# Kernel tuning notes

Hardware: AMD Instinct MI355X
Metric: run time of the kernel (lower is better)

Reference implementation:

```python
import jax, jax.numpy as jnp
import numpy as np

H = W = 56
HID = 384
B = 16

def dct_mat(N):
    # Orthonormal DCT-II matrix: X = D @ x, idct via D.T
    n = jnp.arange(N, dtype=jnp.float32)
    k = jnp.arange(N, dtype=jnp.float32)[:, None]
    D = jnp.cos(jnp.pi * (2.0 * n + 1.0) * k / (2.0 * N)) * jnp.sqrt(2.0 / N)
    D = D.at[0].multiply(1.0 / jnp.sqrt(2.0))
    return D

def setup_inputs() -> dict:
    key = jax.random.key(0)
    ks = jax.random.split(key, 16)
    s = 0.02
    return {
        "x": jax.random.normal(ks[0], (B, HID, H, W), dtype=jnp.float32),
        "freq_embed": jax.random.normal(ks[1], (H, W, HID), dtype=jnp.float32),
        "dw_w": jax.random.normal(ks[2], (HID, 1, 3, 3), dtype=jnp.float32) * s,
        "dw_b": jnp.zeros((HID,), jnp.float32),
        "lin_w": jax.random.normal(ks[3], (2 * HID, HID), dtype=jnp.float32) * s,
        "lin_b": jnp.zeros((2 * HID,), jnp.float32),
        "vel_w": jax.random.normal(ks[4], (HID, HID), dtype=jnp.float32) * s,
        "vel_b": jnp.zeros((HID,), jnp.float32),
        "tok_w": jax.random.normal(ks[5], (HID, HID), dtype=jnp.float32) * s,
        "tok_b": jnp.zeros((HID,), jnp.float32),
        "ln_g": jnp.ones((HID,), jnp.float32),
        "ln_b": jnp.zeros((HID,), jnp.float32),
        "out_w": jax.random.normal(ks[6], (HID, HID), dtype=jnp.float32) * s,
        "out_b": jnp.zeros((HID,), jnp.float32),
        "c": jnp.ones((1,), jnp.float32),
        "alpha": jnp.ones((1,), jnp.float32) * 0.1,
    }

def reference(x, freq_embed, dw_w, dw_b, lin_w, lin_b, vel_w, vel_b,
              tok_w, tok_b, ln_g, ln_b, out_w, out_b, c, alpha):
    Bn, C, Hh, Ww = x.shape
    # depthwise 3x3 conv, padding=1
    x = jax.lax.conv_general_dilated(
        x, dw_w, (1, 1), 'SAME',
        dimension_numbers=('NCHW', 'OIHW', 'NCHW'),
        feature_group_count=C) + dw_b[None, :, None, None]
    xl = jnp.transpose(x, (0, 2, 3, 1))            # [B,H,W,C]
    xz = xl @ lin_w.T + lin_b                      # [B,H,W,2C]
    xg, z = jnp.split(xz, 2, axis=-1)
    DH, DW_ = dct_mat(Hh), dct_mat(Ww)
    x_ch = jnp.transpose(xg, (0, 3, 1, 2))         # [B,C,H,W]
    x_u0 = jnp.einsum('ih,jw,bchw->bcij', DH, DW_, x_ch)
    x_vel = xg @ vel_w.T + vel_b                   # [B,H,W,C]
    x_v0 = jnp.einsum('ih,jw,bchw->bcij', DH, DW_, jnp.transpose(x_vel, (0, 3, 1, 2)))
    # decay map exp(-(n^2+m^2)) on linspace(0,pi)
    wn = jnp.linspace(0.0, jnp.pi, Hh + 1)[:Hh][:, None]
    wm = jnp.linspace(0.0, jnp.pi, Ww + 1)[:Ww][None, :]
    decay = jnp.exp(-(wn ** 2 + wm ** 2))[None, None]
    x_u0 = x_u0 * decay
    x_v0 = x_v0 * decay
    # wave modulation from freq embedding (shared across batch)
    t = jax.nn.relu(freq_embed @ tok_w.T + tok_b)  # [H,W,C]
    t = jnp.transpose(t, (2, 0, 1))[None]          # [1,C,H,W]
    eps = 1e-6
    cos_t = jnp.cos(c[0] * t)
    sin_t = jnp.sin(c[0] * t) / (c[0] + eps)
    final = cos_t * x_u0 + sin_t * (x_v0 + 0.5 * alpha[0] * x_u0)
    x_final = jnp.einsum('hi,wj,bchw->bcij', DH, DW_, final)  # IDCT2D
    y = jnp.transpose(x_final, (0, 2, 3, 1))       # [B,H,W,C]
    mu = jnp.mean(y, axis=-1, keepdims=True)
    var = jnp.mean((y - mu) ** 2, axis=-1, keepdims=True)
    yn = (y - mu) / jnp.sqrt(var + 1e-5) * ln_g + ln_b
    gated = yn * jax.nn.silu(z)                    # [B,H,W,C]
    out = gated @ out_w.T + out_b
    return jnp.transpose(out, (0, 3, 1, 2))        # [B,C,H,W]
```

## Files before the change

kernel.cpp:

```cpp
#include <hip/hip_runtime.h>
#include <math.h>

#define HH 56
#define WS_W 56
#define HWS 3136
#define CD 384
#define BB 16
#define NROW (BB*HWS)
#define SLOT ((size_t)NROW*CD)

typedef __attribute__((ext_vector_type(8))) short bf16x8;
typedef __attribute__((ext_vector_type(4))) float f32x4;

__device__ inline ushort f2bf(float v) {
  uint u = __float_as_uint(v);
  uint r = (u + 0x7fffu + ((u >> 16) & 1u)) >> 16;
  return (ushort)r;
}
__device__ inline float bf2f(ushort h) { return __uint_as_float((uint)h << 16); }

__device__ inline void gl16(const void* g, void* l) {
  __builtin_amdgcn_global_load_lds(
      (const __attribute__((address_space(1))) void*)g,
      (__attribute__((address_space(3))) void*)l,
      16, 0, 0);
}

__global__ void prep_d_k(float* __restrict__ D) {
  for (int idx = threadIdx.x; idx < HH*HH; idx += blockDim.x) {
    int k = idx / HH, n = idx % HH;
    double v = cos(3.14159265358979323846 * (2.0*n + 1.0) * k / (2.0*HH)) * sqrt(2.0/HH);
    if (k == 0) v *= 0.70710678118654752440;
    D[idx] = (float)v;
  }
}

__global__ void prep_pack_k(const float* __restrict__ Dm, ushort* __restrict__ Dpk) {
  for (int idx = threadIdx.x; idx < 2*4096; idx += 256) {
    int o = idx >> 12, e = idx & 4095;
    int mg = e >> 10, rem = e & 1023;
    int j = rem & 7, km = rem >> 3;
    int koct = km >> 4, m16 = km & 15;
    int m = mg*16 + m16, k = koct*8 + j;
    float v = 0.f;
    if (m < 56 && k < 56) v = o ? Dm[k*56 + m] : Dm[m*56 + k];
    ushort h = f2bf(v);
    Dpk[o*8192 + e] = h;
    Dpk[o*8192 + 4096 + e] = f2bf(v - bf2f(h));
  }
}

__global__ __launch_bounds__(256) void split_w_k(
    const float* __restrict__ W, ushort* __restrict__ hi,
    ushort* __restrict__ lo, int nelem) {
  int i = blockIdx.x*256 + threadIdx.x;
  if (i >= nelem) return;
  float v = W[i];
  ushort h = f2bf(v);
  hi[i] = h;
  lo[i] = f2bf(v - bf2f(h));
}

__global__ __launch_bounds__(256) void conv_k(
    const float* __restrict__ x, const float* __restrict__ dww,
    const float* __restrict__ dwb, ushort* __restrict__ xc)
{
  __shared__ float xs[3][58][33];
  __shared__ float wgt[32][9];
  __shared__ float wb[32];
  int t = threadIdx.x;
  int c0 = blockIdx.x * 32, h = blockIdx.y, b = blockIdx.z;
  for (int idx = t; idx < 1344; idx += 256) {
    int wq = idx % 14, rem = idx / 14;
    int dy = rem % 3, ch = rem / 3;
    int gh = h + dy - 1;
    float4 v = {0.f, 0.f, 0.f, 0.f};
    if (gh >= 0 && gh < HH)
      v = *(const float4*)(x + (((size_t)b*CD + c0 + ch)*HH + gh)*WS_W + wq*4);
    int wp = wq*4 + 1;
    xs[dy][wp+0][ch] = v.x;
    xs[dy][wp+1][ch] = v.y;
    xs[dy][wp+2][ch] = v.z;
    xs[dy][wp+3][ch] = v.w;
  }
  if (t < 192) {
    int e = t & 1, dy = (t >> 1) % 3, ch = t / 6;
    xs[dy][e*57][ch] = 0.f;
  }
  for (int idx = t; idx < 288; idx += 256)
    wgt[idx/9][idx%9] = dww[(size_t)(c0 + idx/9)*9 + idx%9];
  if (t < 32) wb[t] = dwb[c0 + t];
  __syncthreads();
  int ch = t & 31, wq8 = t >> 5;
  #pragma unroll
  for (int wwi = 0; wwi < 7; ++wwi) {
    int w = wwi*8 + wq8;
    float acc = wb[ch];
    #pragma unroll
    for (int dy = 0; dy < 3; ++dy)
      #pragma unroll
      for (int dx = 0; dx < 3; ++dx)
        acc = fmaf(wgt[ch][dy*3+dx], xs[dy][w+dx][ch], acc);
    size_t oi = ((size_t)b*HWS + h*WS_W + w)*CD + c0 + ch;
    ushort hh = f2bf(acc);
    xc[oi] = hh;
    xc[SLOT + oi] = f2bf(acc - bf2f(hh));
  }
}

template<int EPI>
__global__ __launch_bounds__(256) void gemm_k(
    const float* __restrict__ A, const float* __restrict__ Bw,
    const float* __restrict__ bias, float* __restrict__ out0,
    float* __restrict__ out1, const float* __restrict__ cptr)
{
  __shared__ float As[16][68];
  __shared__ float Bs[16][68];
  int t = threadIdx.x;
  int col0 = blockIdx.x * 64;
  int row0 = blockIdx.y * 64;
  int lr = t >> 2, lk = (t & 3) * 4;
  const float* Ap = A + (size_t)(row0 + lr)*CD + lk;
  const float* Bp = Bw + (size_t)(col0 + lr)*CD + lk;
  float acc[4][4] = {};
  int tx = t & 15, ty = t >> 4;
  for (int k0 = 0; k0 < CD; k0 += 16) {
    float4 av = *(const float4*)(Ap + k0);
    float4 bv = *(const float4*)(Bp + k0);
    __syncthreads();
    As[lk+0][lr] = av.x; As[lk+1][lr] = av.y; As[lk+2][lr] = av.z; As[lk+3][lr] = av.w;
    Bs[lk+0][lr] = bv.x; Bs[lk+1][lr] = bv.y; Bs[lk+2][lr] = bv.z; Bs[lk+3][lr] = bv.w;
    __syncthreads();
    #pragma unroll
    for (int k = 0; k < 16; ++k) {
      float4 a4 = *(const float4*)&As[k][ty*4];
      float4 b4 = *(const float4*)&Bs[k][tx*4];
      float aa[4] = {a4.x, a4.y, a4.z, a4.w};
      float bbv[4] = {b4.x, b4.y, b4.z, b4.w};
      #pragma unroll
      for (int i = 0; i < 4; ++i)
        #pragma unroll
        for (int j = 0; j < 4; ++j)
          acc[i][j] = fmaf(aa[i], bbv[j], acc[i][j]);
    }
  }
  float cs = 0.f;
  if constexpr (EPI == 2) cs = cptr[0];
  #pragma unroll
  for (int i = 0; i < 4; ++i) {
    int r = row0 + ty*4 + i;
    #pragma unroll
    for (int j = 0; j < 4; ++j) {
      int cg = col0 + tx*4 + j;
      float v = acc[i][j];
      if constexpr (EPI == 2) {
        v += bias[cg];
        v = fmaxf(v, 0.f);
        int pi = r / 56, pj = r % 56;
        float wn = 3.14159265358979323846f/56.f * (float)pi;
        float wm = 3.14159265358979323846f/56.f * (float)pj;
        float dec = expf(-(wn*wn + wm*wm));
        out0[(size_t)r*CD + cg] = cosf(cs*v)*dec;
        out1[(size_t)r*CD + cg] = sinf(cs*v)/(cs + 1e-6f)*dec;
      }
    }
  }
}

template<int EPI>
__global__ __launch_bounds__(256, 2) void mgemm_k(
    const ushort* __restrict__ Ah_g, const ushort* __restrict__ Al_g,
    const ushort* __restrict__ Wh, const ushort* __restrict__ Wl,
    const float* __restrict__ bias,
    float* __restrict__ out0, float* __restrict__ out1,
    const ushort* __restrict__ UinH, const float* __restrict__ cosD,
    const float* __restrict__ sinD, const float* __restrict__ velb,
    const float* __restrict__ alphap)
{
  __shared__ char smem[32768];
  int t = threadIdx.x;
  int nwg = gridDim.x * gridDim.y;
  int wgid = blockIdx.y * gridDim.x + blockIdx.x;
  int cpx = nwg >> 3;
  int sw = (wgid & 7) * cpx + (wgid >> 3);
  int col0 = (sw % gridDim.x) * 128;
  int row0 = (sw / gridDim.x) * 128;

  int r = t >> 1, half = t & 1;
  int n = r & 15, rt = r >> 4, q0 = half * 2;
  const ushort* Ahp = Ah_g + (size_t)(row0 + r)*CD + half*16;
  const ushort* Alp = Al_g + (size_t)(row0 + r)*CD + half*16;
  const ushort* Bhp = Wh + (size_t)(col0 + r)*CD + half*16;
  const ushort* Blp = Wl + (size_t)(col0 + r)*CD + half*16;
  int aoff0 = rt*1024 + (q0*16 + n)*16;
  int aoff1 = rt*1024 + ((q0+1)*16 + n)*16;
  int boff0 = 16384 + aoff0, boff1 = 16384 + aoff1;
  int wid = t >> 6, lane = t & 63;
  int wr = wid >> 1, wc = wid & 1;
  f32x4 acc[4][4];
  #pragma unroll
  for (int i = 0; i < 4; ++i)
    #pragma unroll
    for (int j = 0; j < 4; ++j)
      acc[i][j] = (f32x4){0.f, 0.f, 0.f, 0.f};

  for (int k0 = 0; k0 < CD; k0 += 32) {
    uint4 fh0 = *(const uint4*)(Ahp + k0);
    uint4 fh1 = *(const uint4*)(Ahp + k0 + 8);
    uint4 fl0 = *(const uint4*)(Alp + k0);
    uint4 fl1 = *(const uint4*)(Alp + k0 + 8);
    uint4 bh0 = *(const uint4*)(Bhp + k0);
    uint4 bh1 = *(const uint4*)(Bhp + k0 + 8);
    uint4 bl0 = *(const uint4*)(Blp + k0);
    uint4 bl1 = *(const uint4*)(Blp + k0 + 8);
    __syncthreads();
    *(uint4*)(smem + aoff0)        = fh0;
    *(uint4*)(smem + aoff0 + 8192) = fl0;
    *(uint4*)(smem + aoff1)        = fh1;
    *(uint4*)(smem + aoff1 + 8192) = fl1;
    *(uint4*)(smem + boff0)        = bh0;
    *(uint4*)(smem + boff0 + 8192) = bl0;
    *(uint4*)(smem + boff1)        = bh1;
    *(uint4*)(smem + boff1 + 8192) = bl1;
    __syncthreads();
    bf16x8 Ah[4], Al[4], Bh[4], Bl[4];
    #pragma unroll
    for (int i = 0; i < 4; ++i) {
      int ao = (wr*4 + i)*1024 + lane*16;
      Ah[i] = *(const bf16x8*)(smem + ao);
      Al[i] = *(const bf16x8*)(smem + ao + 8192);
      int bo = 16384 + (wc*4 + i)*1024 + lane*16;
      Bh[i] = *(const bf16x8*)(smem + bo);
      Bl[i] = *(const bf16x8*)(smem + bo + 8192);
    }
    #pragma unroll
    for (int i = 0; i < 4; ++i)
      #pragma unroll
      for (int j = 0; j < 4; ++j) {
        acc[i][j] = __builtin_amdgcn_mfma_f32_16x16x32_bf16(Ah[i], Bh[j], acc[i][j], 0, 0, 0);
        acc[i][j] = __builtin_amdgcn_mfma_f32_16x16x32_bf16(Ah[i], Bl[j], acc[i][j], 0, 0, 0);
        acc[i][j] = __builtin_amdgcn_mfma_f32_16x16x32_bf16(Al[i], Bh[j], acc[i][j], 0, 0, 0);
      }
  }

  int nn = lane & 15, qq = lane >> 4;
  float ahalf = 0.f;
  if constexpr (EPI == 1) ahalf = 0.5f * alphap[0];
  #pragma unroll
  for (int i = 0; i < 4; ++i) {
    #pragma unroll
    for (int j = 0; j < 4; ++j) {
      #pragma unroll
      for (int reg = 0; reg < 4; ++reg) {
        int rg = row0 + wr*64 + i*16 + qq*4 + reg;
        int cg = col0 + wc*64 + j*16 + nn;
        float v = acc[i][j][reg];
        if constexpr (EPI == 0) {
          v += bias[cg];
          if (cg < CD) out0[(size_t)rg*CD + cg] = v;
          else         out1[(size_t)rg*CD + cg - CD] = v;
        } else if constexpr (EPI == 1) {
          int p = rg % HWS;
          size_t uidx = (size_t)rg*CD + cg;
          float u  = bf2f(UinH[uidx]) + bf2f(UinH[SLOT + uidx]);
          float cd = cosD[(size_t)p*CD + cg];
          float sd = sinD[(size_t)p*CD + cg];
          if (p == 0) v += 56.f * velb[cg];
          out0[uidx] = cd*u + sd*(v + ahalf*u);
        } else {
          v += bias[cg];
          int bidx = rg / HWS, hw = rg % HWS;
          out0[((size_t)bidx*CD + cg)*HWS + hw] = v;
        }
      }
    }
  }
}

template<int OSPLIT>
__global__ __launch_bounds__(256, 3) void dmm_k(
    const float* __restrict__ in, float* __restrict__ outf,
    const ushort* __restrict__ Dpk, int NBT, int RS, size_t BSTR)
{
  __shared__ char smem[49152];
  int t = threadIdx.x;
  int flat = blockIdx.x;
  int sw = (flat & 7) * 336 + (flat >> 3);
  int batch = sw / NBT, nt0 = sw - batch*NBT;
  int n0 = nt0 * 128;
  const float* inb = in + (size_t)batch*BSTR;
  int wid = t >> 6, lane = t & 63;

  {
    const char* src = (const char*)Dpk;
    #pragma unroll
    for (int i = 0; i < 4; ++i)
      gl16(src + wid*4096 + i*1024 + lane*16,
           smem + 32768 + wid*4096 + i*1024);
  }

  {
    int koct = t >> 5, c4 = (t & 31) * 4;
    float4 fr[8];
    if (koct < 7) {
      #pragma unroll
      for (int j = 0; j < 8; ++j)
        fr[j] = *(const float4*)(inb + (size_t)(koct*8 + j)*RS + n0 + c4);
    } else {
      #pragma unroll
      for (int j = 0; j < 8; ++j) fr[j] = (float4){0.f,0.f,0.f,0.f};
    }
    #pragma unroll
    for (int c = 0; c < 4; ++c) {
      ushort hs[8], ls[8];
      #pragma unroll
      for (int j = 0; j < 8; ++j) {
        float v = ((const float*)&fr[j])[c];
        hs[j] = f2bf(v);
        ls[j] = f2bf(v - bf2f(hs[j]));
      }
      uint4 hv, lv;
      hv.x = hs[0]|((uint)hs[1]<<16); hv.y = hs[2]|((uint)hs[3]<<16);
      hv.z = hs[4]|((uint)hs[5]<<16); hv.w = hs[6]|((uint)hs[7]<<16);
      lv.x = ls[0]|((uint)ls[1]<<16); lv.y = ls[2]|((uint)ls[3]<<16);
      lv.z = ls[4]|((uint)ls[5]<<16); lv.w = ls[6]|((uint)ls[7]<<16);
      int nn = c4 + c;
      int off = (nn >> 4)*2048 + (koct*16 + ((nn & 15) ^ koct))*16;
      *(uint4*)(smem + off)         = hv;
      *(uint4*)(smem + 16384 + off) = lv;
    }
  }
  __syncthreads();

  int mg = wid;
  bf16x8 Ah[2], Al[2];
  #pragma unroll
  for (int ks = 0; ks < 2; ++ks) {
    int ao = 32768 + mg*2048 + ((ks*4 + (lane>>4))*16 + (lane&15))*16;
    Ah[ks] = *(const bf16x8*)(smem + ao);
    Al[ks] = *(const bf16x8*)(smem + ao + 8192);
  }
  f32x4 acc[8];
  #pragma unroll
  for (int nt = 0; nt < 8; ++nt) acc[nt] = (f32x4){0.f,0.f,0.f,0.f};
  #pragma unroll
  for (int nt = 0; nt < 8; ++nt) {
    #pragma unroll
    for (int ks = 0; ks < 2; ++ks) {
      int koctr = ks*4 + (lane>>4);
      int bo = nt*2048 + (koctr*16 + ((lane & 15) ^ koctr))*16;
      bf16x8 Bh = *(const bf16x8*)(smem + bo);
      bf16x8 Bl = *(const bf16x8*)(smem + bo + 16384);
      acc[nt] = __builtin_amdgcn_mfma_f32_16x16x32_bf16(Ah[ks], Bh, acc[nt], 0, 0, 0);
      acc[nt] = __builtin_amdgcn_mfma_f32_16x16x32_bf16(Ah[ks], Bl, acc[nt], 0, 0, 0);
      acc[nt] = __builtin_amdgcn_mfma_f32_16x16x32_bf16(Al[ks], Bh, acc[nt], 0, 0, 0);
      acc[nt] = __builtin_amdgcn_mfma_f32_16x16x32_bf16(Al[ks], Bl, acc[nt], 0, 0, 0);
    }
  }

  int q = lane >> 4, n16 = lane & 15;
  #pragma unroll
  for (int nt = 0; nt < 8; ++nt) {
    #pragma unroll
    for (int reg = 0; reg < 4; ++reg) {
      int m = mg*16 + q*4 + reg;
      if (m < 56) {
        size_t addr = (size_t)batch*BSTR + (size_t)m*RS + n0 + nt*16 + n16;
        float v = acc[nt][reg];
        if constexpr (OSPLIT == 0) {
          outf[addr] = v;
        } else {
          ushort* oh = (ushort*)outf;
          ushort hh = f2bf(v);
          oh[addr] = hh;
          oh[SLOT + addr] = f2bf(v - bf2f(hh));
        }
      }
    }
  }
}

__global__ __launch_bounds__(256) void ln_gate_k(
    const float* __restrict__ Y, const float* __restrict__ Z,
    const float* __restrict__ g, const float* __restrict__ be,
    ushort* __restrict__ out)
{
  int lane = threadIdx.x & 63, wv = threadIdx.x >> 6;
  size_t r = (size_t)blockIdx.x*4 + wv;
  const float* y = Y + r*CD;
  float v[6];
  float s = 0.f;
  #pragma unroll
  for (int q = 0; q < 6; ++q) { v[q] = y[lane + 64*q]; s += v[q]; }
  #pragma unroll
  for (int off = 32; off > 0; off >>= 1) s += __shfl_xor(s, off, 64);
  float mu = s * (1.f/384.f);
  float s2 = 0.f;
  #pragma unroll
  for (int q = 0; q < 6; ++q) { float d = v[q]-mu; s2 += d*d; }
  #pragma unroll
  for (int off = 32; off > 0; off >>= 1) s2 += __shfl_xor(s2, off, 64);
  float rs = 1.f / sqrtf(s2*(1.f/384.f) + 1e-5f);
  #pragma unroll
  for (int q = 0; q < 6; ++q) {
    int c = lane + 64*q;
    float yn = (v[q]-mu)*rs*g[c] + be[c];
    float zv = Z[r*CD + c];
    float sz = zv / (1.f + expf(-zv));
    float gv = yn*sz;
    ushort hh = f2bf(gv);
    out[r*CD + c] = hh;
    out[SLOT + r*CD + c] = f2bf(gv - bf2f(hh));
  }
}

extern "C" void kernel_launch(void* const* d_in, const int* in_sizes, int n_in,
                              void* d_out, int out_size, void* d_ws, size_t ws_size,
                              hipStream_t stream) {
  const float* x     = (const float*)d_in[0];
  const float* fe    = (const float*)d_in[1];
  const float* dw_w  = (const float*)d_in[2];
  const float* dw_b  = (const float*)d_in[3];
  const float* lin_w = (const float*)d_in[4];
  const float* lin_b = (const float*)d_in[5];
  const float* vel_w = (const float*)d_in[6];
  const float* vel_b = (const float*)d_in[7];
  const float* tok_w = (const float*)d_in[8];
  const float* tok_b = (const float*)d_in[9];
  const float* ln_g  = (const float*)d_in[10];
  const float* ln_b  = (const float*)d_in[11];
  const float* out_w = (const float*)d_in[12];
  const float* out_b = (const float*)d_in[13];
  const float* cp    = (const float*)d_in[14];
  const float* ap    = (const float*)d_in[15];

  float* ws    = (float*)d_ws;
  float* slotA = ws;
  float* slotB = ws + SLOT;
  float* slotC = ws + 2*SLOT;
  float* Dm    = ws + 3*SLOT;
  float* cosD  = Dm + 3136;
  float* sinD  = cosD + (size_t)HWS*CD;
  ushort* whi  = (ushort*)(sinD + (size_t)HWS*CD);
  ushort* wlo  = whi + 589824;
  ushort* Dpk  = wlo + 589824;

  ushort* xcH = (ushort*)slotA;
  ushort* UH  = (ushort*)slotB;
  ushort* GH  = (ushort*)slotB;

  prep_d_k<<<1, 256, 0, stream>>>(Dm);
  prep_pack_k<<<1, 256, 0, stream>>>(Dm, Dpk);
  split_w_k<<<1152, 256, 0, stream>>>(lin_w, whi,          wlo,          294912);
  split_w_k<<< 576, 256, 0, stream>>>(vel_w, whi + 294912, wlo + 294912, 147456);
  split_w_k<<< 576, 256, 0, stream>>>(out_w, whi + 442368, wlo + 442368, 147456);

  conv_k<<<dim3(12, 56, 16), 256, 0, stream>>>(x, dw_w, dw_b, xcH);
  gemm_k<2><<<dim3(6, 49), 256, 0, stream>>>(fe, tok_w, tok_b, cosD, sinD, cp);
  mgemm_k<0><<<dim3(6, 392), 256, 0, stream>>>(xcH, xcH + SLOT, whi, wlo, lin_b,
      slotB, slotC, nullptr, nullptr, nullptr, nullptr, nullptr);
  dmm_k<0><<<2688, 256, 0, stream>>>(slotB, slotA, Dpk,        168, 21504, (size_t)1204224);
  dmm_k<1><<<2688, 256, 0, stream>>>(slotA, slotB, Dpk,          3,   384, (size_t)21504);
  mgemm_k<1><<<dim3(3, 392), 256, 0, stream>>>(UH, UH + SLOT, whi + 294912, wlo + 294912,
      nullptr, slotA, nullptr, UH, cosD, sinD, vel_b, ap);
  dmm_k<0><<<2688, 256, 0, stream>>>(slotA, slotB, Dpk + 8192, 168, 21504, (size_t)1204224);
  dmm_k<0><<<2688, 256, 0, stream>>>(slotB, slotA, Dpk + 8192,   3,   384, (size_t)21504);
  ln_gate_k<<<12544, 256, 0, stream>>>(slotA, slotC, ln_g, ln_b, GH);
  mgemm_k<3><<<dim3(3, 392), 256, 0, stream>>>(GH, GH + SLOT, whi + 442368, wlo + 442368,
      out_b, (float*)d_out, nullptr, nullptr, nullptr, nullptr, nullptr, nullptr);
}
```

Before: 678.8 us.

## Fuse final IDCT column pass with LayerNorm gating; transpose output GEMM operands

```diff
diff --git a/kernel.cpp b/kernel.cpp
--- a/kernel.cpp
+++ b/kernel.cpp
@@ -183,8 +183,10 @@
   int wgid = blockIdx.y * gridDim.x + blockIdx.x;
   int cpx = nwg >> 3;
   int sw = (wgid & 7) * cpx + (wgid >> 3);
-  int col0 = (sw % gridDim.x) * 128;
-  int row0 = (sw / gridDim.x) * 128;
+  int colT = sw % gridDim.x, rowT = sw / gridDim.x;
+  int col0, row0;
+  if constexpr (EPI == 3) { row0 = colT * 128; col0 = rowT * 128; }
+  else                    { col0 = colT * 128; row0 = rowT * 128; }
 
   int r = t >> 1, half = t & 1;
   int n = r & 15, rt = r >> 4, q0 = half * 2;
@@ -252,25 +254,29 @@
     for (int j = 0; j < 4; ++j) {
       #pragma unroll
       for (int reg = 0; reg < 4; ++reg) {
-        int rg = row0 + wr*64 + i*16 + qq*4 + reg;
-        int cg = col0 + wc*64 + j*16 + nn;
         float v = acc[i][j][reg];
-        if constexpr (EPI == 0) {
-          v += bias[cg];
-          if (cg < CD) out0[(size_t)rg*CD + cg] = v;
-          else         out1[(size_t)rg*CD + cg - CD] = v;
-        } else if constexpr (EPI == 1) {
-          int p = rg % HWS;
-          size_t uidx = (size_t)rg*CD + cg;
-          float u  = bf2f(UinH[uidx]) + bf2f(UinH[SLOT + uidx]);
-          float cd = cosD[(size_t)p*CD + cg];
-          float sd = sinD[(size_t)p*CD + cg];
-          if (p == 0) v += 56.f * velb[cg];
-          out0[uidx] = cd*u + sd*(v + ahalf*u);
+        if constexpr (EPI == 3) {
+          int m  = row0 + wr*64 + i*16 + qq*4 + reg;
+          int ng = col0 + wc*64 + j*16 + nn;
+          v += bias[m];
+          int bidx = ng / HWS, hw = ng % HWS;
+          out0[((size_t)bidx*CD + m)*HWS + hw] = v;
         } else {
-          v += bias[cg];
-          int bidx = rg / HWS, hw = rg % HWS;
-          out0[((size_t)bidx*CD + cg)*HWS + hw] = v;
+          int rg = row0 + wr*64 + i*16 + qq*4 + reg;
+          int cg = col0 + wc*64 + j*16 + nn;
+          if constexpr (EPI == 0) {
+            v += bias[cg];
+            if (cg < CD) out0[(size_t)rg*CD + cg] = v;
+            else         out1[(size_t)rg*CD + cg - CD] = v;
+          } else {
+            int p = rg % HWS;
+            size_t uidx = (size_t)rg*CD + cg;
+            float u  = bf2f(UinH[uidx]) + bf2f(UinH[SLOT + uidx]);
+            float cd = cosD[(size_t)p*CD + cg];
+            float sd = sinD[(size_t)p*CD + cg];
+            if (p == 0) v += 56.f * velb[cg];
+            out0[uidx] = cd*u + sd*(v + ahalf*u);
+          }
         }
       }
     }
@@ -380,37 +386,122 @@
   }
 }
 
-__global__ __launch_bounds__(256) void ln_gate_k(
-    const float* __restrict__ Y, const float* __restrict__ Z,
+__global__ __launch_bounds__(256, 1) void dmm_ln_k(
+    const float* __restrict__ in, const float* __restrict__ Z,
     const float* __restrict__ g, const float* __restrict__ be,
-    ushort* __restrict__ out)
+    ushort* __restrict__ outg, const ushort* __restrict__ Dpk)
 {
-  int lane = threadIdx.x & 63, wv = threadIdx.x >> 6;
-  size_t r = (size_t)blockIdx.x*4 + wv;
-  const float* y = Y + r*CD;
-  float v[6];
-  float s = 0.f;
-  #pragma unroll
-  for (int q = 0; q < 6; ++q) { v[q] = y[lane + 64*q]; s += v[q]; }
-  #pragma unroll
-  for (int off = 32; off > 0; off >>= 1) s += __shfl_xor(s, off, 64);
-  float mu = s * (1.f/384.f);
-  float s2 = 0.f;
-  #pragma unroll
-  for (int q = 0; q < 6; ++q) { float d = v[q]-mu; s2 += d*d; }
-  #pragma unroll
-  for (int off = 32; off > 0; off >>= 1) s2 += __shfl_xor(s2, off, 64);
-  float rs = 1.f / sqrtf(s2*(1.f/384.f) + 1e-5f);
-  #pragma unroll
-  for (int q = 0; q < 6; ++q) {
-    int c = lane + 64*q;
-    float yn = (v[q]-mu)*rs*g[c] + be[c];
-    float zv = Z[r*CD + c];
-    float sz = zv / (1.f + expf(-zv));
-    float gv = yn*sz;
-    ushort hh = f2bf(gv);
-    out[r*CD + c] = hh;
-    out[SLOT + r*CD + c] = f2bf(gv - bf2f(hh));
+  __shared__ char smem[117760];
+  int t = threadIdx.x;
+  int flat = blockIdx.x;
+  int bt = (flat & 7) * 112 + (flat >> 3);
+  const float* inb = in + (size_t)bt * 21504;
+  int wid = t >> 6, lane = t & 63;
+
+  {
+    const char* src = (const char*)Dpk;
+    #pragma unroll
+    for (int i = 0; i < 4; ++i)
+      gl16(src + wid*4096 + i*1024 + lane*16,
+           smem + 98304 + wid*4096 + i*1024);
+  }
+  if (t < 96) {
+    ((float4*)(smem + 114688))[t] = ((const float4*)g)[t];
+    ((float4*)(smem + 116224))[t] = ((const float4*)be)[t];
+  }
+  for (int ch = 0; ch < 3; ++ch) {
+    int koct = t >> 5, c4 = (t & 31) * 4;
+    float4 fr[8];
+    if (koct < 7) {
+      #pragma unroll
+      for (int j = 0; j < 8; ++j)
+        fr[j] = *(const float4*)(inb + (size_t)(koct*8 + j)*CD + ch*128 + c4);
+    } else {
+      #pragma unroll
+      for (int j = 0; j < 8; ++j) fr[j] = (float4){0.f,0.f,0.f,0.f};
+    }
+    #pragma unroll
+    for (int c = 0; c < 4; ++c) {
+      ushort hs[8], ls[8];
+      #pragma unroll
+      for (int j = 0; j < 8; ++j) {
+        float v = ((const float*)&fr[j])[c];
+        hs[j] = f2bf(v);
+        ls[j] = f2bf(v - bf2f(hs[j]));
+      }
+      uint4 hv, lv;
+      hv.x = hs[0]|((uint)hs[1]<<16); hv.y = hs[2]|((uint)hs[3]<<16);
+      hv.z = hs[4]|((uint)hs[5]<<16); hv.w = hs[6]|((uint)hs[7]<<16);
+      lv.x = ls[0]|((uint)ls[1]<<16); lv.y = ls[2]|((uint)ls[3]<<16);
+      lv.z = ls[4]|((uint)ls[5]<<16); lv.w = ls[6]|((uint)ls[7]<<16);
+      int nn = c4 + c;
+      int off = ch*16384 + (nn >> 4)*2048 + (koct*16 + ((nn & 15) ^ koct))*16;
+      *(uint4*)(smem + off)         = hv;
+      *(uint4*)(smem + 49152 + off) = lv;
+    }
+  }
+  __syncthreads();
+
+  int mg = wid;
+  bf16x8 Ah[2], Al[2];
+  #pragma unroll
+  for (int ks = 0; ks < 2; ++ks) {
+    int ao = 98304 + mg*2048 + ((ks*4 + (lane>>4))*16 + (lane&15))*16;
+    Ah[ks] = *(const bf16x8*)(smem + ao);
+    Al[ks] = *(const bf16x8*)(smem + ao + 8192);
+  }
+  f32x4 acc[24];
+  #pragma unroll
+  for (int nt = 0; nt < 24; ++nt) acc[nt] = (f32x4){0.f,0.f,0.f,0.f};
+  #pragma unroll
+  for (int nt = 0; nt < 24; ++nt) {
+    #pragma unroll
+    for (int ks = 0; ks < 2; ++ks) {
+      int koctr = ks*4 + (lane>>4);
+      int bo = (nt >> 3)*16384 + (nt & 7)*2048 + (koctr*16 + ((lane & 15) ^ koctr))*16;
+      bf16x8 Bh = *(const bf16x8*)(smem + bo);
+      bf16x8 Bl = *(const bf16x8*)(smem + bo + 49152);
+      acc[nt] = __builtin_amdgcn_mfma_f32_16x16x32_bf16(Ah[ks], Bh, acc[nt], 0, 0, 0);
+      acc[nt] = __builtin_amdgcn_mfma_f32_16x16x32_bf16(Ah[ks], Bl, acc[nt], 0, 0, 0);
+      acc[nt] = __builtin_amdgcn_mfma_f32_16x16x32_bf16(Al[ks], Bh, acc[nt], 0, 0, 0);
+      acc[nt] = __builtin_amdgcn_mfma_f32_16x16x32_bf16(Al[ks], Bl, acc[nt], 0, 0, 0);
+    }
+  }
+
+  int q = lane >> 4, n16 = lane & 15;
+  int b = bt / 56, h = bt % 56;
+  size_t rowbase = ((size_t)b*HWS + (size_t)h*56) * CD;
+  const float* gs = (const float*)(smem + 114688);
+  const float* bs = (const float*)(smem + 116224);
+  #pragma unroll
+  for (int reg = 0; reg < 4; ++reg) {
+    int m = mg*16 + q*4 + reg;
+    float s = 0.f;
+    #pragma unroll
+    for (int nt = 0; nt < 24; ++nt) s += acc[nt][reg];
+    #pragma unroll
+    for (int off = 8; off > 0; off >>= 1) s += __shfl_xor(s, off, 64);
+    float mu = s * (1.f/384.f);
+    float s2 = 0.f;
+    #pragma unroll
+    for (int nt = 0; nt < 24; ++nt) { float d = acc[nt][reg] - mu; s2 += d*d; }
+    #pragma unroll
+    for (int off = 8; off > 0; off >>= 1) s2 += __shfl_xor(s2, off, 64);
+    float rs = 1.f / sqrtf(s2*(1.f/384.f) + 1e-5f);
+    if (m < 56) {
+      size_t rb = rowbase + (size_t)m*CD;
+      #pragma unroll
+      for (int nt = 0; nt < 24; ++nt) {
+        int c = nt*16 + n16;
+        float yn = (acc[nt][reg] - mu)*rs*gs[c] + bs[c];
+        float zv = Z[rb + c];
+        float sz = zv / (1.f + expf(-zv));
+        float gv = yn*sz;
+        ushort hh = f2bf(gv);
+        outg[rb + c] = hh;
+        outg[SLOT + rb + c] = f2bf(gv - bf2f(hh));
+      }
+    }
   }
 }
 
@@ -447,7 +538,7 @@
 
   ushort* xcH = (ushort*)slotA;
   ushort* UH  = (ushort*)slotB;
-  ushort* GH  = (ushort*)slotB;
+  ushort* GH  = (ushort*)slotA;
 
   prep_d_k<<<1, 256, 0, stream>>>(Dm);
   prep_pack_k<<<1, 256, 0, stream>>>(Dm, Dpk);
@@ -464,8 +555,7 @@
   mgemm_k<1><<<dim3(3, 392), 256, 0, stream>>>(UH, UH + SLOT, whi + 294912, wlo + 294912,
       nullptr, slotA, nullptr, UH, cosD, sinD, vel_b, ap);
   dmm_k<0><<<2688, 256, 0, stream>>>(slotA, slotB, Dpk + 8192, 168, 21504, (size_t)1204224);
-  dmm_k<0><<<2688, 256, 0, stream>>>(slotB, slotA, Dpk + 8192,   3,   384, (size_t)21504);
-  ln_gate_k<<<12544, 256, 0, stream>>>(slotA, slotC, ln_g, ln_b, GH);
-  mgemm_k<3><<<dim3(3, 392), 256, 0, stream>>>(GH, GH + SLOT, whi + 442368, wlo + 442368,
+  dmm_ln_k<<<896, 256, 0, stream>>>(slotB, slotC, ln_g, ln_b, GH, Dpk + 8192);
+  mgemm_k<3><<<dim3(3, 392), 256, 0, stream>>>(whi + 442368, wlo + 442368, GH, GH + SLOT,
       out_b, (float*)d_out, nullptr, nullptr, nullptr, nullptr, nullptr, nullptr);
 }
```

After: 706.2 us. 4.0% more time.
